# Performance work log

Hardware: AMD Instinct MI355X
Metric: run time of the kernel (lower is better)

The kernel has to match this reference:

```python
import jax, jax.numpy as jnp
import numpy as np


def setup_inputs() -> dict:
    key = jax.random.key(0)
    ks = jax.random.split(key, 7)
    B, C, H, W = 8, 256, 64, 64
    C8 = C // 8
    s = 0.05
    return {
        "x": jax.random.normal(ks[0], (B, C, H, W), dtype=jnp.float32),
        "wq": jax.random.normal(ks[1], (C8, C), dtype=jnp.float32) * s,
        "bq": jax.random.normal(ks[2], (C8,), dtype=jnp.float32) * s,
        "wk": jax.random.normal(ks[3], (C8, C), dtype=jnp.float32) * s,
        "bk": jax.random.normal(ks[4], (C8,), dtype=jnp.float32) * s,
        "wv": jax.random.normal(ks[5], (C, C), dtype=jnp.float32) * s,
        "bv": jax.random.normal(ks[6], (C,), dtype=jnp.float32) * s,
    }


def reference(x, wq, bq, wk, bk, wv, bv):
    B, C, H, W = x.shape
    xf = x.reshape(B, C, H * W)                      # [B, C, N]
    # conv1x1 projections (per-position linear over channels)
    f = jnp.einsum('oc,bcn->bon', wq, xf) + bq[None, :, None]   # [B, C/8, N]
    g = jnp.einsum('oc,bcn->bon', wk, xf) + bk[None, :, None]   # [B, C/8, N]
    h = jnp.einsum('oc,bcn->bon', wv, xf) + bv[None, :, None]   # [B, C,   N]
    # scores[b, n, m] = sum_c f[b,c,n] * g[b,c,m]  == bmm(f^T, g)
    scores = jnp.einsum('bcn,bcm->bnm', f, g)        # [B, N, N]
    # NOTE: original uses softmax over dim=1 (the f/query-position axis)
    beta = jax.nn.softmax(scores, axis=1)            # [B, N, N]
    # o[b, c, m] = sum_n h[b,c,n] * beta[b,n,m]  == bmm(h, beta)
    o = jnp.einsum('bcn,bnm->bcm', h, beta)          # [B, C, N]
    return o.reshape(B, C, H, W)
```

## Files before the change

kernel.cpp:

```cpp
#include <hip/hip_runtime.h>
#include <hip/hip_bf16.h>

typedef __bf16 bf16_t;
typedef __bf16 bf16x8 __attribute__((ext_vector_type(8)));
typedef __bf16 bf16x4 __attribute__((ext_vector_type(4)));
typedef float  f32x4  __attribute__((ext_vector_type(4)));

#define NB  8
#define NC  256
#define NC8 32
#define NN  4096
#define XS  264

#define MFMA16(a, b, c) __builtin_amdgcn_mfma_f32_16x16x32_bf16((a), (b), (c), 0, 0, 0)

__global__ __launch_bounds__(256) void cvt_all(const float* __restrict__ wq,
                                               const float* __restrict__ wk,
                                               const float* __restrict__ wv,
                                               bf16_t* __restrict__ wqb,
                                               bf16_t* __restrict__ wkb,
                                               bf16_t* __restrict__ wvb) {
    int i = blockIdx.x * 256 + threadIdx.x;
    const float* src; bf16_t* dst; int off;
    if (i < 2048)      { src = wq; dst = wqb; off = i; }
    else if (i < 4096) { src = wk; dst = wkb; off = i - 2048; }
    else               { src = wv; dst = wvb; off = i - 4096; }
    float4 v = reinterpret_cast<const float4*>(src)[off];
    bf16x4 o;
    o[0] = (bf16_t)v.x; o[1] = (bf16_t)v.y; o[2] = (bf16_t)v.z; o[3] = (bf16_t)v.w;
    reinterpret_cast<bf16x4*>(dst)[off] = o;
}

__global__ __launch_bounds__(256) void xpose(const float* __restrict__ x,
                                             bf16_t* __restrict__ xt) {
    __shared__ bf16_t tile[64][72];
    __shared__ bf16_t xs[64 * XS];

    const int bx = blockIdx.x;
    const int b  = bx >> 6;
    const int n0 = (bx & 63) * 64;
    const int t  = threadIdx.x;

    const int cl  = t >> 4;
    const int nl  = (t & 15) * 4;
    const int nb_ = t >> 3;
    const int cl2 = (t & 7) * 8;

    float4 xv[16];
#pragma unroll
    for (int cp = 0; cp < 4; ++cp)
#pragma unroll
        for (int p = 0; p < 4; ++p)
            xv[4 * cp + p] = *reinterpret_cast<const float4*>(
                x + ((size_t)b * NC + 64 * cp + cl + 16 * p) * NN + n0 + nl);

    for (int cp = 0; cp < 4; ++cp) {
#pragma unroll
        for (int p = 0; p < 4; ++p) {
            const int cc = cl + 16 * p;
            float4 v = xv[4 * cp + p];
            bf16x4 bv4;
            bv4[0] = (bf16_t)v.x; bv4[1] = (bf16_t)v.y; bv4[2] = (bf16_t)v.z; bv4[3] = (bf16_t)v.w;
            *reinterpret_cast<bf16x4*>(&tile[cc][nl]) = bv4;
        }
        __syncthreads();
#pragma unroll
        for (int p = 0; p < 2; ++p) {
            const int nn = nb_ + 32 * p;
            bf16x8 v;
            for (int i = 0; i < 8; ++i) v[i] = tile[cl2 + i][nn];
            *reinterpret_cast<bf16x8*>(&xs[nn * XS + 64 * cp + cl2]) = v;
        }
        __syncthreads();
    }

    const int row = t >> 5;
    const int ch  = t & 31;
#pragma unroll
    for (int p = 0; p < 8; ++p) {
        const int rr = row + 8 * p;
        bf16x8 v = *reinterpret_cast<const bf16x8*>(&xs[rr * XS + ch * 8]);
        *reinterpret_cast<bf16x8*>(xt + ((size_t)b * NN + n0 + rr) * NC + ch * 8) = v;
    }
}

__global__ __launch_bounds__(256) void projmm(const bf16_t* __restrict__ xt,
                                              const bf16_t* __restrict__ wq,
                                              const float* __restrict__ bq,
                                              const bf16_t* __restrict__ wk,
                                              const float* __restrict__ bk,
                                              const bf16_t* __restrict__ wv,
                                              const float* __restrict__ bv,
                                              bf16_t* __restrict__ ft,
                                              bf16_t* __restrict__ gt,
                                              bf16_t* __restrict__ h) {
    const int bx = blockIdx.x;
    const int b  = bx >> 6;
    const int n0 = (bx & 63) * 64;
    const int t  = threadIdx.x;
    const int w    = t >> 6;
    const int lane = t & 63;
    const int q    = lane >> 4;
    const int r    = lane & 15;

    const bf16_t* xb = xt + ((size_t)b * NN + n0) * NC;

    {
        const bf16_t* xrow = xb + (size_t)(16 * w + r) * NC;
        f32x4 accq[2], acck[2];
        for (int ot = 0; ot < 2; ++ot) {
            accq[ot] = (f32x4){0.f, 0.f, 0.f, 0.f};
            acck[ot] = (f32x4){0.f, 0.f, 0.f, 0.f};
        }
        bf16x8 a_c  = *reinterpret_cast<const bf16x8*>(xrow + 8 * q);
        bf16x8 fq_c[2], fk_c[2];
#pragma unroll
        for (int ot = 0; ot < 2; ++ot) {
            fq_c[ot] = *reinterpret_cast<const bf16x8*>(wq + (size_t)(16 * ot + r) * NC + 8 * q);
            fk_c[ot] = *reinterpret_cast<const bf16x8*>(wk + (size_t)(16 * ot + r) * NC + 8 * q);
        }
        for (int k0 = 0; k0 < NC; k0 += 32) {
            const int kn = (k0 + 32 < NC) ? k0 + 32 : 0;
            bf16x8 a_n = *reinterpret_cast<const bf16x8*>(xrow + kn + 8 * q);
            bf16x8 fq_n[2], fk_n[2];
#pragma unroll
            for (int ot = 0; ot < 2; ++ot) {
                fq_n[ot] = *reinterpret_cast<const bf16x8*>(wq + (size_t)(16 * ot + r) * NC + kn + 8 * q);
                fk_n[ot] = *reinterpret_cast<const bf16x8*>(wk + (size_t)(16 * ot + r) * NC + kn + 8 * q);
            }
#pragma unroll
            for (int ot = 0; ot < 2; ++ot) {
                accq[ot] = MFMA16(a_c, fq_c[ot], accq[ot]);
                acck[ot] = MFMA16(a_c, fk_c[ot], acck[ot]);
            }
            a_c = a_n;
#pragma unroll
            for (int ot = 0; ot < 2; ++ot) { fq_c[ot] = fq_n[ot]; fk_c[ot] = fk_n[ot]; }
        }
        for (int ot = 0; ot < 2; ++ot) {
            const int o = 16 * ot + r;
            const float biq = bq[o];
            const float bik = bk[o];
            for (int i = 0; i < 4; ++i) {
                const int n = n0 + 16 * w + 4 * q + i;
                ft[((size_t)b * NN + n) * NC8 + o] = (bf16_t)(accq[ot][i] + biq);
                gt[((size_t)b * NN + n) * NC8 + o] = (bf16_t)(acck[ot][i] + bik);
            }
        }
    }

    f32x4 vacc[4][4];
    for (int ct = 0; ct < 4; ++ct)
        for (int nt = 0; nt < 4; ++nt) vacc[ct][nt] = (f32x4){0.f, 0.f, 0.f, 0.f};

    bf16x8 wv_c[4], bfr_c[4];
#pragma unroll
    for (int ct = 0; ct < 4; ++ct)
        wv_c[ct] = *reinterpret_cast<const bf16x8*>(
            wv + (size_t)(64 * ct + 16 * w + r) * NC + 8 * q);
#pragma unroll
    for (int nt = 0; nt < 4; ++nt)
        bfr_c[nt] = *reinterpret_cast<const bf16x8*>(xb + (size_t)(16 * nt + r) * NC + 8 * q);

    for (int k0 = 0; k0 < NC; k0 += 32) {
        const int kn = (k0 + 32 < NC) ? k0 + 32 : 0;
        bf16x8 wv_n[4], bfr_n[4];
#pragma unroll
        for (int ct = 0; ct < 4; ++ct)
            wv_n[ct] = *reinterpret_cast<const bf16x8*>(
                wv + (size_t)(64 * ct + 16 * w + r) * NC + kn + 8 * q);
#pragma unroll
        for (int nt = 0; nt < 4; ++nt)
            bfr_n[nt] = *reinterpret_cast<const bf16x8*>(xb + (size_t)(16 * nt + r) * NC + kn + 8 * q);
#pragma unroll
        for (int ct = 0; ct < 4; ++ct)
#pragma unroll
            for (int nt = 0; nt < 4; ++nt)
                vacc[ct][nt] = MFMA16(wv_c[ct], bfr_c[nt], vacc[ct][nt]);
#pragma unroll
        for (int ct = 0; ct < 4; ++ct) wv_c[ct] = wv_n[ct];
#pragma unroll
        for (int nt = 0; nt < 4; ++nt) bfr_c[nt] = bfr_n[nt];
    }
    for (int ct = 0; ct < 4; ++ct) {
        for (int nt = 0; nt < 4; ++nt) {
            const int n32 = (n0 >> 5) + (nt >> 1);
            const int dn  = 16 * (nt & 1) + r;
            for (int i = 0; i < 4; ++i) {
                const int c = 64 * ct + 16 * w + 4 * q + i;
                h[(((size_t)b * 128 + n32) * NC + c) * 32 + dn] = (bf16_t)(vacc[ct][nt][i] + bv[c]);
            }
        }
    }
}

#define O_STEP(HU, HL, KC, LOFF)                                               \
    {                                                                          \
        _Pragma("unroll")                                                      \
        for (int ct = 0; ct < 2; ++ct)                                         \
            HL[ct] = *reinterpret_cast<const bf16x8*>(                         \
                hrow[ct] + (size_t)(LOFF) * 256);                              \
        bf16x8 pf[4];                                                          \
        _Pragma("unroll")                                                      \
        for (int mt = 0; mt < 4; ++mt) {                                       \
            const int row = 16 * mt + r;                                       \
            pf[mt] = *reinterpret_cast<const bf16x8*>(                         \
                &Pb[(row << 7) + (((4 * (KC) + q) ^ rq) << 3)]);               \
        }                                                                      \
        _Pragma("unroll")                                                      \
        for (int ct = 0; ct < 2; ++ct)                                         \
            _Pragma("unroll")                                                  \
            for (int mt = 0; mt < 4; ++mt)                                     \
                acc[ct][mt] = MFMA16(HU[ct], pf[mt], acc[ct][mt]);             \
    }

__global__ __launch_bounds__(512, 4) void attn(const bf16_t* __restrict__ ft,
                                               const bf16_t* __restrict__ gt,
                                               const bf16_t* __restrict__ h,
                                               float* __restrict__ out) {
    __shared__ bf16_t P[2 * 64 * 128];
    __shared__ float  l_lds[64];

    const int bx = blockIdx.x;
    const int b  = bx & 7;
    const int m0 = (bx >> 3) * 64;
    const int tid  = threadIdx.x;
    const int w    = tid >> 6;
    const int lane = tid & 63;
    const int q    = lane >> 4;
    const int r    = lane & 15;
    const int rq   = r & 7;

    if (tid < 64) l_lds[tid] = 0.f;

    bf16x8 qf[4];
#pragma unroll
    for (int mt = 0; mt < 4; ++mt)
        qf[mt] = *reinterpret_cast<const bf16x8*>(
            gt + ((size_t)b * NN + m0 + 16 * mt + r) * NC8 + 8 * q);

    f32x4 acc[2][4];
#pragma unroll
    for (int ct = 0; ct < 2; ++ct)
#pragma unroll
        for (int mt = 0; mt < 4; ++mt) acc[ct][mt] = (f32x4){0.f, 0.f, 0.f, 0.f};
    float lp[4] = {0.f, 0.f, 0.f, 0.f};

    const bf16_t* fb = ft + (size_t)b * NN * NC8;
    const bf16_t* hb = h + (size_t)b * 128 * NC * 32;
    const f32x4 zero = (f32x4){0.f, 0.f, 0.f, 0.f};

    const bf16_t* hrow[2];
#pragma unroll
    for (int ct = 0; ct < 2; ++ct)
        hrow[ct] = hb + (size_t)(32 * w + 16 * ct + r) * 32 + 8 * q;
    const bf16_t* fptr = fb + (size_t)(16 * w + r) * NC8 + 8 * q;

    f32x4 s[4];
    {
        bf16x8 a0 = *reinterpret_cast<const bf16x8*>(fptr);
#pragma unroll
        for (int mt = 0; mt < 4; ++mt) s[mt] = MFMA16(a0, qf[mt], zero);
    }
    bf16x8 h0[2], h1[2];
#pragma unroll
    for (int ct = 0; ct < 2; ++ct)
        h0[ct] = *reinterpret_cast<const bf16x8*>(hrow[ct]);

    for (int ii = 0; ii < 32; ++ii) {
        bf16_t* Pb = &P[(ii & 1) << 13];
        const int nb = ii * 128;
        const int nld = (ii + 1 < 32 ? ii + 1 : 31) * 128;

        bf16x8 af0 = *reinterpret_cast<const bf16x8*>(fptr + (size_t)nld * NC8);

#pragma unroll
        for (int mt = 0; mt < 4; ++mt) {
            float e0 = __expf(s[mt][0]);
            float e1 = __expf(s[mt][1]);
            float e2 = __expf(s[mt][2]);
            float e3 = __expf(s[mt][3]);
            lp[mt] += (e0 + e1) + (e2 + e3);
            bf16x4 pv;
            pv[0] = (bf16_t)e0; pv[1] = (bf16_t)e1; pv[2] = (bf16_t)e2; pv[3] = (bf16_t)e3;
            const int row  = 16 * mt + r;
            const int nblk = 2 * w + (q >> 1);
            *reinterpret_cast<bf16x4*>(
                &Pb[(row << 7) + ((nblk ^ rq) << 3) + 4 * (q & 1)]) = pv;
        }

        asm volatile("s_waitcnt lgkmcnt(0)" ::: "memory");
        __builtin_amdgcn_sched_barrier(0);
        __builtin_amdgcn_s_barrier();
        __builtin_amdgcn_sched_barrier(0);

        const int nbn = (ii + 1 < 32 ? nb + 128 : nb);
        __builtin_amdgcn_s_setprio(1);
        O_STEP(h0, h1, 0, nb + 32);
        O_STEP(h1, h0, 1, nb + 64);
        O_STEP(h0, h1, 2, nb + 96);
        O_STEP(h1, h0, 3, nbn);

#pragma unroll
        for (int mt = 0; mt < 4; ++mt) s[mt] = MFMA16(af0, qf[mt], zero);
        __builtin_amdgcn_s_setprio(0);
    }

    __syncthreads();
#pragma unroll
    for (int mt = 0; mt < 4; ++mt) {
        float v = lp[mt];
        v += __shfl_xor(v, 16);
        v += __shfl_xor(v, 32);
        if (q == 0) atomicAdd(&l_lds[16 * mt + r], v);
    }
    __syncthreads();

#pragma unroll
    for (int ct = 0; ct < 2; ++ct) {
#pragma unroll
        for (int mt = 0; mt < 4; ++mt) {
            const int m = m0 + 16 * mt + r;
            const float linv = 1.0f / l_lds[16 * mt + r];
#pragma unroll
            for (int i = 0; i < 4; ++i) {
                const int c = 32 * w + 16 * ct + 4 * q + i;
                out[((size_t)b * NC + c) * NN + m] = acc[ct][mt][i] * linv;
            }
        }
    }
}

extern "C" void kernel_launch(void* const* d_in, const int* in_sizes, int n_in,
                              void* d_out, int out_size, void* d_ws, size_t ws_size,
                              hipStream_t stream) {
    const float* x  = (const float*)d_in[0];
    const float* wq = (const float*)d_in[1];
    const float* bq = (const float*)d_in[2];
    const float* wk = (const float*)d_in[3];
    const float* bk = (const float*)d_in[4];
    const float* wv = (const float*)d_in[5];
    const float* bv = (const float*)d_in[6];
    float* out = (float*)d_out;

    bf16_t* ft  = (bf16_t*)d_ws;
    bf16_t* gt  = ft + (size_t)NB * NN * NC8;
    bf16_t* hb  = gt + (size_t)NB * NN * NC8;
    bf16_t* wqb = hb + (size_t)NB * NC * NN;
    bf16_t* wkb = wqb + (size_t)NC8 * NC;
    bf16_t* wvb = wkb + (size_t)NC8 * NC;

    bf16_t* xT = (bf16_t*)out;

    cvt_all<<<80, 256, 0, stream>>>(wq, wk, wv, wqb, wkb, wvb);
    xpose<<<NB * (NN / 64), 256, 0, stream>>>(x, xT);
    projmm<<<NB * (NN / 64), 256, 0, stream>>>(xT, wqb, bq, wkb, bk, wvb, bv, ft, gt, hb);
    attn<<<NB * (NN / 64), 512, 0, stream>>>(ft, gt, hb, out);
}
```

Before: 203.1 us.

## Store x^T and weights in 16x32 MFMA-panel tiled layout for coalesced fragment loads

The weight conversion and the x transpose kernels now write bf16 data into a blocked layout of 16-row by 32-column panels, so each MFMA fragment (16 rows x 32 k) is one contiguous 1 KB block. The projection kernel reads its A/B fragments from these panels with simple offsets, so each wavefront's fragment load covers contiguous memory instead of 16 rows strided by 512 bytes. This targets cache-line and TLB efficiency in projmm. The attention kernels are unaffected because they read ft/gt/h, whose layouts are unchanged.

```diff
diff --git a/kernel.cpp b/kernel.cpp
--- a/kernel.cpp
+++ b/kernel.cpp
@@ -13,6 +13,7 @@
 #define XS  264
 
 #define MFMA16(a, b, c) __builtin_amdgcn_mfma_f32_16x16x32_bf16((a), (b), (c), 0, 0, 0)
+
 
 __global__ __launch_bounds__(256) void cvt_all(const float* __restrict__ wq,
                                                const float* __restrict__ wk,
@@ -26,9 +27,13 @@
     else if (i < 4096) { src = wk; dst = wkb; off = i - 2048; }
     else               { src = wv; dst = wvb; off = i - 4096; }
     float4 v = reinterpret_cast<const float4*>(src)[off];
-    bf16x4 o;
-    o[0] = (bf16_t)v.x; o[1] = (bf16_t)v.y; o[2] = (bf16_t)v.z; o[3] = (bf16_t)v.w;
-    reinterpret_cast<bf16x4*>(dst)[off] = o;
+    const int e = off * 4;
+    const int o = e >> 8;
+    const int k = e & 255;
+    const size_t d = (size_t)((o >> 4) * 8 + (k >> 5)) * 512 + (o & 15) * 32 + (k & 31);
+    bf16x4 ov;
+    ov[0] = (bf16_t)v.x; ov[1] = (bf16_t)v.y; ov[2] = (bf16_t)v.z; ov[3] = (bf16_t)v.w;
+    *reinterpret_cast<bf16x4*>(dst + d) = ov;
 }
 
 __global__ __launch_bounds__(256) void xpose(const float* __restrict__ x,
@@ -76,11 +81,15 @@
 
     const int row = t >> 5;
     const int ch  = t & 31;
+    const int kp  = ch >> 2;
+    const int c8  = (ch & 3) * 8;
 #pragma unroll
     for (int p = 0; p < 8; ++p) {
         const int rr = row + 8 * p;
         bf16x8 v = *reinterpret_cast<const bf16x8*>(&xs[rr * XS + ch * 8]);
-        *reinterpret_cast<bf16x8*>(xt + ((size_t)b * NN + n0 + rr) * NC + ch * 8) = v;
+        const int np = (n0 >> 4) + (rr >> 4);
+        *reinterpret_cast<bf16x8*>(
+            xt + ((size_t)(b * 256 + np) * 8 + kp) * 512 + (rr & 15) * 32 + c8) = v;
     }
 }
 
@@ -103,30 +112,33 @@
     const int q    = lane >> 4;
     const int r    = lane & 15;
 
-    const bf16_t* xb = xt + ((size_t)b * NN + n0) * NC;
+    const int fo = r * 32 + 8 * q;
+    const bf16_t* xpb = xt + (size_t)b * 256 * 8 * 512;
 
     {
-        const bf16_t* xrow = xb + (size_t)(16 * w + r) * NC;
+        const bf16_t* apan = xpb + (size_t)((n0 >> 4) + w) * 4096 + fo;
+        const bf16_t* wqp  = wq + fo;
+        const bf16_t* wkp  = wk + fo;
         f32x4 accq[2], acck[2];
         for (int ot = 0; ot < 2; ++ot) {
             accq[ot] = (f32x4){0.f, 0.f, 0.f, 0.f};
             acck[ot] = (f32x4){0.f, 0.f, 0.f, 0.f};
         }
-        bf16x8 a_c  = *reinterpret_cast<const bf16x8*>(xrow + 8 * q);
+        bf16x8 a_c = *reinterpret_cast<const bf16x8*>(apan);
         bf16x8 fq_c[2], fk_c[2];
 #pragma unroll
         for (int ot = 0; ot < 2; ++ot) {
-            fq_c[ot] = *reinterpret_cast<const bf16x8*>(wq + (size_t)(16 * ot + r) * NC + 8 * q);
-            fk_c[ot] = *reinterpret_cast<const bf16x8*>(wk + (size_t)(16 * ot + r) * NC + 8 * q);
-        }
-        for (int k0 = 0; k0 < NC; k0 += 32) {
-            const int kn = (k0 + 32 < NC) ? k0 + 32 : 0;
-            bf16x8 a_n = *reinterpret_cast<const bf16x8*>(xrow + kn + 8 * q);
+            fq_c[ot] = *reinterpret_cast<const bf16x8*>(wqp + ot * 4096);
+            fk_c[ot] = *reinterpret_cast<const bf16x8*>(wkp + ot * 4096);
+        }
+        for (int kp = 0; kp < 8; ++kp) {
+            const int kn = (kp + 1 < 8) ? kp + 1 : 0;
+            bf16x8 a_n = *reinterpret_cast<const bf16x8*>(apan + kn * 512);
             bf16x8 fq_n[2], fk_n[2];
 #pragma unroll
             for (int ot = 0; ot < 2; ++ot) {
-                fq_n[ot] = *reinterpret_cast<const bf16x8*>(wq + (size_t)(16 * ot + r) * NC + kn + 8 * q);
-                fk_n[ot] = *reinterpret_cast<const bf16x8*>(wk + (size_t)(16 * ot + r) * NC + kn + 8 * q);
+                fq_n[ot] = *reinterpret_cast<const bf16x8*>(wqp + ot * 4096 + kn * 512);
+                fk_n[ot] = *reinterpret_cast<const bf16x8*>(wkp + ot * 4096 + kn * 512);
             }
 #pragma unroll
             for (int ot = 0; ot < 2; ++ot) {
@@ -153,25 +165,26 @@
     for (int ct = 0; ct < 4; ++ct)
         for (int nt = 0; nt < 4; ++nt) vacc[ct][nt] = (f32x4){0.f, 0.f, 0.f, 0.f};
 
+    const bf16_t* wvp  = wv + (size_t)w * 4096 + fo;
+    const bf16_t* vpan = xpb + (size_t)(n0 >> 4) * 4096 + fo;
+
     bf16x8 wv_c[4], bfr_c[4];
 #pragma unroll
     for (int ct = 0; ct < 4; ++ct)
-        wv_c[ct] = *reinterpret_cast<const bf16x8*>(
-            wv + (size_t)(64 * ct + 16 * w + r) * NC + 8 * q);
+        wv_c[ct] = *reinterpret_cast<const bf16x8*>(wvp + (size_t)ct * 16384);
 #pragma unroll
     for (int nt = 0; nt < 4; ++nt)
-        bfr_c[nt] = *reinterpret_cast<const bf16x8*>(xb + (size_t)(16 * nt + r) * NC + 8 * q);
-
-    for (int k0 = 0; k0 < NC; k0 += 32) {
-        const int kn = (k0 + 32 < NC) ? k0 + 32 : 0;
+        bfr_c[nt] = *reinterpret_cast<const bf16x8*>(vpan + (size_t)nt * 4096);
+
+    for (int kp = 0; kp < 8; ++kp) {
+        const int kn = (kp + 1 < 8) ? kp + 1 : 0;
         bf16x8 wv_n[4], bfr_n[4];
 #pragma unroll
         for (int ct = 0; ct < 4; ++ct)
-            wv_n[ct] = *reinterpret_cast<const bf16x8*>(
-                wv + (size_t)(64 * ct + 16 * w + r) * NC + kn + 8 * q);
+            wv_n[ct] = *reinterpret_cast<const bf16x8*>(wvp + (size_t)ct * 16384 + kn * 512);
 #pragma unroll
         for (int nt = 0; nt < 4; ++nt)
-            bfr_n[nt] = *reinterpret_cast<const bf16x8*>(xb + (size_t)(16 * nt + r) * NC + kn + 8 * q);
+            bfr_n[nt] = *reinterpret_cast<const bf16x8*>(vpan + (size_t)nt * 4096 + kn * 512);
 #pragma unroll
         for (int ct = 0; ct < 4; ++ct)
 #pragma unroll
```

Result: faster. 196.0 us (-3.5%).
